# Kernel optimization log

Measured on AMD Instinct MI355X. Metric: run time of the kernel, lower is better.

The kernel has to match this reference:

```python
import jax, jax.numpy as jnp
import numpy as np

B, T, S, D, V = 8, 128, 400, 512, 50000
EPS_LN = 1e-6

def setup_inputs() -> dict:
    key = jax.random.key(0)
    ks = jax.random.split(key, 10)
    a = jax.random.uniform(ks[0], (B, T, S), dtype=jnp.float32)
    attn_weights = a / jnp.sum(a, axis=-1, keepdims=True)  # row-stochastic like softmax attention
    return {
        'x': jax.random.normal(ks[1], (B, T, D), dtype=jnp.float32),
        'x_t': jax.random.normal(ks[2], (B, T, D), dtype=jnp.float32),
        'memory': jax.random.normal(ks[3], (B, S, D), dtype=jnp.float32),
        'attn_weights': attn_weights,
        'src': jax.random.randint(ks[4], (B, S), 0, V),
        'norm_a': jnp.ones((D,), jnp.float32),
        'norm_b': jnp.zeros((D,), jnp.float32),
        'proj_w': jax.random.normal(ks[5], (V, D), dtype=jnp.float32) * (1.0 / np.sqrt(D)),
        'proj_b': jnp.zeros((V,), jnp.float32),
        'wh_w': jax.random.normal(ks[6], (1, D), dtype=jnp.float32) * (1.0 / np.sqrt(D)),
        'wh_b': jnp.zeros((1,), jnp.float32),
        'ws_w': jax.random.normal(ks[7], (1, D), dtype=jnp.float32) * (1.0 / np.sqrt(D)),
        'ws_b': jnp.zeros((1,), jnp.float32),
        'wx_w': jax.random.normal(ks[8], (1, D), dtype=jnp.float32) * (1.0 / np.sqrt(D)),
        'wx_b': jnp.zeros((1,), jnp.float32),
        'bptr': jnp.zeros((1, 1), jnp.float32),
    }

def _layer_norm(x, a, b):
    mu = jnp.mean(x, axis=-1, keepdims=True)
    sd = jnp.std(x, axis=-1, keepdims=True)
    return a * (x - mu) / (sd + EPS_LN) + b

def reference(x, x_t, memory, attn_weights, src, norm_a, norm_b, proj_w, proj_b,
              wh_w, wh_b, ws_w, ws_b, wx_w, wx_b, bptr):
    # generation distribution over vocab: [B,T,V]
    dec_dist = jnp.einsum('btd,vd->btv', _layer_norm(x, norm_a, norm_b), proj_w) + proj_b
    # context vector h_t = attn @ memory: [B,T,D]
    h_t = jnp.einsum('bts,bsd->btd', attn_weights, memory)
    # p_gen gate: [B,T,1]
    logits = (jnp.einsum('btd,od->bto', h_t, wh_w) + wh_b
              + jnp.einsum('btd,od->bto', x, ws_w) + ws_b
              + jnp.einsum('btd,od->bto', x_t, wx_w) + wx_b
              + bptr[0, 0])
    p_gen = jax.nn.sigmoid(logits)
    # copy distribution via scatter_add of attention mass onto source token ids
    b_idx = jnp.arange(B)[:, None, None]
    t_idx = jnp.arange(T)[None, :, None]
    v_idx = src[:, None, :]  # broadcast over T -> [B,T,S] index
    enc_attn_dist = jnp.zeros((B, T, V), dtype=dec_dist.dtype).at[b_idx, t_idx, v_idx].add(attn_weights)
    out = jnp.log(p_gen * jax.nn.softmax(dec_dist, axis=-1) + (1.0 - p_gen) * enc_attn_dist + 1e-12)
    return out, p_gen
```

## Files before the change

### kernel.cpp

```cpp
#include <hip/hip_runtime.h>
#include <hip/hip_bf16.h>
#include <cstdint>

#define B_  8
#define T_  128
#define S_  400
#define D_  512
#define V_  50000
#define M_  (B_*T_)
#define EPS_LN 1e-6f

typedef __bf16 bf16x8 __attribute__((ext_vector_type(8)));
typedef float  f32x4  __attribute__((ext_vector_type(4)));
typedef unsigned short u16;
typedef unsigned short u16x4 __attribute__((ext_vector_type(4)));
typedef unsigned short u16x8 __attribute__((ext_vector_type(8)));

__device__ __forceinline__ float bf2f(u16 u) {
    union { unsigned i; float f; } c; c.i = ((unsigned)u) << 16; return c.f;
}
__device__ __forceinline__ u16 f2bf(float f) {
    union { float f; unsigned i; } c; c.f = f;
    unsigned i = c.i;
    unsigned r = (i + 0x7FFFu + ((i >> 16) & 1u)) >> 16;
    return (u16)r;
}

__device__ __forceinline__ float bsum(float v, float* sb) {
    #pragma unroll
    for (int o = 32; o; o >>= 1) v += __shfl_xor(v, o);
    __syncthreads();
    if ((threadIdx.x & 63) == 0) sb[threadIdx.x >> 6] = v;
    __syncthreads();
    return sb[0] + sb[1] + sb[2] + sb[3];
}
__device__ __forceinline__ float bmax(float v, float* sb) {
    #pragma unroll
    for (int o = 32; o; o >>= 1) v = fmaxf(v, __shfl_xor(v, o));
    __syncthreads();
    if ((threadIdx.x & 63) == 0) sb[threadIdx.x >> 6] = v;
    __syncthreads();
    return fmaxf(fmaxf(sb[0], sb[1]), fmaxf(sb[2], sb[3]));
}

__global__ void k_mw(const float* __restrict__ mem, const float* __restrict__ wh,
                     float* __restrict__ mw) {
    __shared__ float sb[4];
    int row = blockIdx.x;
    const float* mr = mem + (size_t)row * D_;
    int t = threadIdx.x;
    float2 m2 = *(const float2*)(mr + t * 2);
    float2 w2 = *(const float2*)(wh + t * 2);
    float v = m2.x * w2.x + m2.y * w2.y;
    float tot = bsum(v, sb);
    if (t == 0) mw[row] = tot;
}

__global__ void k_wconv(const float* __restrict__ w, u16* __restrict__ wb) {
    size_t i = ((size_t)blockIdx.x * 256 + threadIdx.x) * 8;
    float4 a = *(const float4*)(w + i);
    float4 b = *(const float4*)(w + i + 4);
    u16x8 o;
    o[0] = f2bf(a.x); o[1] = f2bf(a.y); o[2] = f2bf(a.z); o[3] = f2bf(a.w);
    o[4] = f2bf(b.x); o[5] = f2bf(b.y); o[6] = f2bf(b.z); o[7] = f2bf(b.w);
    *(u16x8*)(wb + i) = o;
}

__global__ void k_rows(const float* __restrict__ x, const float* __restrict__ xt,
                       const float* __restrict__ attn, const float* __restrict__ mw,
                       const float* __restrict__ na, const float* __restrict__ nb,
                       const float* __restrict__ wsw, const float* __restrict__ wxw,
                       const float* __restrict__ whb, const float* __restrict__ wsb,
                       const float* __restrict__ wxb, const float* __restrict__ bp,
                       u16* __restrict__ Ab, float* __restrict__ pgen,
                       float* __restrict__ outp) {
    __shared__ float sb[4];
    int row = blockIdx.x;
    int b = row / T_;
    int tid = threadIdx.x;
    const float* xr  = x  + (size_t)row * D_;
    const float* xtr = xt + (size_t)row * D_;
    float2 xv = *(const float2*)(xr + tid * 2);
    float tsx  = bsum(xv.x + xv.y, sb);
    float tsx2 = bsum(xv.x * xv.x + xv.y * xv.y, sb);
    float mu  = tsx / (float)D_;
    float var = fmaxf(tsx2 / (float)D_ - mu * mu, 0.f);
    float rs  = 1.f / (sqrtf(var) + EPS_LN);
    float2 nav = *(const float2*)(na + tid * 2);
    float2 nbv = *(const float2*)(nb + tid * 2);
    u16 a0 = f2bf(nav.x * (xv.x - mu) * rs + nbv.x);
    u16 a1 = f2bf(nav.y * (xv.y - mu) * rs + nbv.y);
    ((unsigned*)(Ab + (size_t)row * D_))[tid] = (unsigned)a0 | ((unsigned)a1 << 16);
    float2 wsv = *(const float2*)(wsw + tid * 2);
    float2 wxv = *(const float2*)(wxw + tid * 2);
    float2 xtv = *(const float2*)(xtr + tid * 2);
    float dot = xv.x * wsv.x + xv.y * wsv.y + xtv.x * wxv.x + xtv.y * wxv.y;
    if (tid < 200) {
        const float* ar  = attn + (size_t)row * S_;
        const float* mwb = mw + b * S_;
        float2 av = *(const float2*)(ar + tid * 2);
        float2 mv = *(const float2*)(mwb + tid * 2);
        dot += av.x * mv.x + av.y * mv.y;
    }
    float tdot = bsum(dot, sb);
    if (tid == 0) {
        float logit = tdot + whb[0] + wsb[0] + wxb[0] + bp[0];
        float p = 1.f / (1.f + __expf(-logit));
        pgen[row] = p;
        outp[row] = p;
    }
}

__global__ __launch_bounds__(256) void k_gemm(const u16* __restrict__ Ab,
                                              const u16* __restrict__ Wb,
                                              const float* __restrict__ projb,
                                              u16* __restrict__ dec) {
    __shared__ __align__(16) u16 As[128 * 32];
    __shared__ __align__(16) u16 Bs[128 * 32];
    int bid = blockIdx.x;
    int xcd = bid & 7, loc = bid >> 3;
    int wg = xcd * 391 + loc;
    int mt = wg & 7, nt = wg >> 3;
    int brow = mt * 128, bcol = nt * 128;
    int tid = threadIdx.x, lane = tid & 63, wv = tid >> 6;
    int wm = wv >> 1, wn = wv & 1;
    int kq = lane >> 4, lr = lane & 15;
    f32x4 acc[4][4] = {};
    for (int kt = 0; kt < 16; ++kt) {
        #pragma unroll
        for (int i = 0; i < 2; ++i) {
            int flat = i * 4096 + tid * 16;
            int r = flat >> 6, kb = flat & 63;
            const u16* ga = Ab + (size_t)(brow + r) * 512 + kt * 32 + (kb >> 1);
            int vr = bcol + r; if (vr >= V_) vr = V_ - 1;
            const u16* gb = Wb + (size_t)vr * 512 + kt * 32 + (kb >> 1);
            __builtin_amdgcn_global_load_lds(
                (const __attribute__((address_space(1))) unsigned*)ga,
                (__attribute__((address_space(3))) unsigned*)((char*)As + flat), 16, 0, 0);
            __builtin_amdgcn_global_load_lds(
                (const __attribute__((address_space(1))) unsigned*)gb,
                (__attribute__((address_space(3))) unsigned*)((char*)Bs + flat), 16, 0, 0);
        }
        __syncthreads();
        bf16x8 af[4], bfr[4];
        const bf16x8* Afp = (const bf16x8*)As;
        const bf16x8* Bfp = (const bf16x8*)Bs;
        #pragma unroll
        for (int m = 0; m < 4; ++m) af[m]  = Afp[(wm * 64 + m * 16 + lr) * 4 + kq];
        #pragma unroll
        for (int n = 0; n < 4; ++n) bfr[n] = Bfp[(wn * 64 + n * 16 + lr) * 4 + kq];
        #pragma unroll
        for (int m = 0; m < 4; ++m)
            #pragma unroll
            for (int n = 0; n < 4; ++n)
                acc[m][n] = __builtin_amdgcn_mfma_f32_16x16x32_bf16(af[m], bfr[n], acc[m][n], 0, 0, 0);
        __syncthreads();
    }
    #pragma unroll
    for (int m = 0; m < 4; ++m) {
        int rbase = brow + wm * 64 + m * 16 + kq * 4;
        #pragma unroll
        for (int n = 0; n < 4; ++n) {
            int col = bcol + wn * 64 + n * 16 + lr;
            if (col < V_) {
                float pb = projb[col];
                #pragma unroll
                for (int i = 0; i < 4; ++i) {
                    int row = rbase + i;
                    dec[(size_t)row * V_ + col] = f2bf(acc[m][n][i] + pb);
                }
            }
        }
    }
}

__global__ void k_stats(const u16* __restrict__ dec, float* __restrict__ base) {
    __shared__ float sb[4];
    int row = blockIdx.x;
    const u16* dr = dec + (size_t)row * V_;
    int tid = threadIdx.x;
    float mx = -1e30f;
    for (int i0 = tid * 8; i0 < V_; i0 += 2048) {
        u16x8 v = *(const u16x8*)(dr + i0);
        #pragma unroll
        for (int j = 0; j < 8; ++j) mx = fmaxf(mx, bf2f(v[j]));
    }
    mx = bmax(mx, sb);
    float s = 0.f;
    for (int i0 = tid * 8; i0 < V_; i0 += 2048) {
        u16x8 v = *(const u16x8*)(dr + i0);
        #pragma unroll
        for (int j = 0; j < 8; ++j) s += __expf(bf2f(v[j]) - mx);
    }
    s = bsum(s, sb);
    if (tid == 0) base[row] = mx + __logf(s);
}

__global__ void k_final(const u16* __restrict__ dec, const float* __restrict__ pgen,
                        const float* __restrict__ base, float* __restrict__ out) {
    int row = blockIdx.y;
    int v0 = blockIdx.x * 1024 + threadIdx.x * 4;
    if (v0 >= V_) return;
    float p  = pgen[row];
    float bs = base[row];
    u16x4 d = *(const u16x4*)(dec + (size_t)row * V_ + v0);
    float4 o;
    o.x = __logf(p * __expf(bf2f(d[0]) - bs) + 1e-12f);
    o.y = __logf(p * __expf(bf2f(d[1]) - bs) + 1e-12f);
    o.z = __logf(p * __expf(bf2f(d[2]) - bs) + 1e-12f);
    o.w = __logf(p * __expf(bf2f(d[3]) - bs) + 1e-12f);
    *(float4*)(out + (size_t)row * V_ + v0) = o;
}

__global__ void k_fix(const int* __restrict__ src, const float* __restrict__ attn,
                      const u16* __restrict__ dec, const float* __restrict__ pgen,
                      const float* __restrict__ base, float* __restrict__ out) {
    int b = blockIdx.x / S_, s = blockIdx.x % S_;
    const int* sr = src + b * S_;
    int v = sr[s];
    for (int s2 = 0; s2 < s; ++s2)
        if (sr[s2] == v) return;
    int t = threadIdx.x;
    float enc = 0.f;
    const float* ar = attn + (size_t)(b * T_ + t) * S_;
    for (int s2 = s; s2 < S_; ++s2)
        if (sr[s2] == v) enc += ar[s2];
    int row = b * T_ + t;
    float p  = pgen[row];
    float bs = base[row];
    float d  = bf2f(dec[(size_t)row * V_ + v]);
    out[(size_t)row * V_ + v] = __logf(p * __expf(d - bs) + (1.f - p) * enc + 1e-12f);
}

extern "C" void kernel_launch(void* const* d_in, const int* in_sizes, int n_in,
                              void* d_out, int out_size, void* d_ws, size_t ws_size,
                              hipStream_t stream) {
    const float* x    = (const float*)d_in[0];
    const float* xt   = (const float*)d_in[1];
    const float* mem  = (const float*)d_in[2];
    const float* attn = (const float*)d_in[3];
    const int*   src  = (const int*)d_in[4];
    const float* na   = (const float*)d_in[5];
    const float* nb   = (const float*)d_in[6];
    const float* pw   = (const float*)d_in[7];
    const float* pb   = (const float*)d_in[8];
    const float* whw  = (const float*)d_in[9];
    const float* whb  = (const float*)d_in[10];
    const float* wsw  = (const float*)d_in[11];
    const float* wsb  = (const float*)d_in[12];
    const float* wxw  = (const float*)d_in[13];
    const float* wxb  = (const float*)d_in[14];
    const float* bp   = (const float*)d_in[15];

    char* ws = (char*)d_ws;
    u16*   Wb   = (u16*)(ws + 0);
    u16*   Ab   = (u16*)(ws + 51200000);
    u16*   dec  = (u16*)(ws + 52248576);
    float* mw   = (float*)(ws + 154648576);
    float* pgen = (float*)(ws + 154661376);
    float* base = (float*)(ws + 154665472);
    float* out  = (float*)d_out;
    float* outp = out + (size_t)M_ * V_;

    k_mw   <<<B_ * S_, 256, 0, stream>>>(mem, whw, mw);
    k_wconv<<<12500, 256, 0, stream>>>(pw, Wb);
    k_rows <<<M_, 256, 0, stream>>>(x, xt, attn, mw, na, nb, wsw, wxw,
                                    whb, wsb, wxb, bp, Ab, pgen, outp);
    k_gemm <<<3128, 256, 0, stream>>>(Ab, Wb, pb, dec);
    k_stats<<<M_, 256, 0, stream>>>(dec, base);
    k_final<<<dim3(49, M_), 256, 0, stream>>>(dec, pgen, base, out);
    k_fix  <<<B_ * S_, 128, 0, stream>>>(src, attn, dec, pgen, base, out);
}
```

Baseline: 276.5 us.

## Fuse softmax row stats into GEMM epilogue and swizzle LDS tile layout

The GEMM epilogue now computes per-row partial max and sum-of-exp for each 128-column tile and writes them to small workspace arrays. A tiny reduce kernel combines these partials into the log-sum-exp base, replacing the stats kernel that re-read the full bf16 logits twice. The LDS tile layout is also reordered so each MFMA fragment is a contiguous per-lane read, and the final kernel handles 8 elements per thread. This adds shuffles and exp work to the GEMM epilogue in exchange for removing a large memory pass.

```diff
diff --git a/kernel.cpp b/kernel.cpp
--- a/kernel.cpp
+++ b/kernel.cpp
@@ -8,12 +8,12 @@
 #define D_  512
 #define V_  50000
 #define M_  (B_*T_)
+#define NT_ 391
 #define EPS_LN 1e-6f
 
 typedef __bf16 bf16x8 __attribute__((ext_vector_type(8)));
 typedef float  f32x4  __attribute__((ext_vector_type(4)));
 typedef unsigned short u16;
-typedef unsigned short u16x4 __attribute__((ext_vector_type(4)));
 typedef unsigned short u16x8 __attribute__((ext_vector_type(8)));
 
 __device__ __forceinline__ float bf2f(u16 u) {
@@ -114,9 +114,13 @@
 __global__ __launch_bounds__(256) void k_gemm(const u16* __restrict__ Ab,
                                               const u16* __restrict__ Wb,
                                               const float* __restrict__ projb,
-                                              u16* __restrict__ dec) {
+                                              u16* __restrict__ dec,
+                                              float* __restrict__ pmax,
+                                              float* __restrict__ psum) {
     __shared__ __align__(16) u16 As[128 * 32];
     __shared__ __align__(16) u16 Bs[128 * 32];
+    __shared__ float smax[2][128];
+    __shared__ float ssum[2][128];
     int bid = blockIdx.x;
     int xcd = bid & 7, loc = bid >> 3;
     int wg = xcd * 391 + loc;
@@ -130,10 +134,13 @@
         #pragma unroll
         for (int i = 0; i < 2; ++i) {
             int flat = i * 4096 + tid * 16;
-            int r = flat >> 6, kb = flat & 63;
-            const u16* ga = Ab + (size_t)(brow + r) * 512 + kt * 32 + (kb >> 1);
-            int vr = bcol + r; if (vr >= V_) vr = V_ - 1;
-            const u16* gb = Wb + (size_t)vr * 512 + kt * 32 + (kb >> 1);
+            int sub = flat >> 10;
+            int l   = (flat >> 4) & 63;
+            int kq2 = l >> 4, lr2 = l & 15;
+            int arow = brow + sub * 16 + lr2;
+            const u16* ga = Ab + (size_t)arow * 512 + kt * 32 + kq2 * 8;
+            int vrow = bcol + sub * 16 + lr2; if (vrow >= V_) vrow = V_ - 1;
+            const u16* gb = Wb + (size_t)vrow * 512 + kt * 32 + kq2 * 8;
             __builtin_amdgcn_global_load_lds(
                 (const __attribute__((address_space(1))) unsigned*)ga,
                 (__attribute__((address_space(3))) unsigned*)((char*)As + flat), 16, 0, 0);
@@ -146,9 +153,9 @@
         const bf16x8* Afp = (const bf16x8*)As;
         const bf16x8* Bfp = (const bf16x8*)Bs;
         #pragma unroll
-        for (int m = 0; m < 4; ++m) af[m]  = Afp[(wm * 64 + m * 16 + lr) * 4 + kq];
-        #pragma unroll
-        for (int n = 0; n < 4; ++n) bfr[n] = Bfp[(wn * 64 + n * 16 + lr) * 4 + kq];
+        for (int m = 0; m < 4; ++m) af[m]  = Afp[(wm * 4 + m) * 64 + lane];
+        #pragma unroll
+        for (int n = 0; n < 4; ++n) bfr[n] = Bfp[(wn * 4 + n) * 64 + lane];
         #pragma unroll
         for (int m = 0; m < 4; ++m)
             #pragma unroll
@@ -156,60 +163,89 @@
                 acc[m][n] = __builtin_amdgcn_mfma_f32_16x16x32_bf16(af[m], bfr[n], acc[m][n], 0, 0, 0);
         __syncthreads();
     }
+    float pbn[4];
+    int   cval[4];
+    #pragma unroll
+    for (int n = 0; n < 4; ++n) {
+        int col = bcol + wn * 64 + n * 16 + lr;
+        cval[n] = (col < V_);
+        pbn[n]  = cval[n] ? projb[col] : 0.f;
+    }
     #pragma unroll
     for (int m = 0; m < 4; ++m) {
-        int rbase = brow + wm * 64 + m * 16 + kq * 4;
-        #pragma unroll
-        for (int n = 0; n < 4; ++n) {
-            int col = bcol + wn * 64 + n * 16 + lr;
-            if (col < V_) {
-                float pb = projb[col];
-                #pragma unroll
-                for (int i = 0; i < 4; ++i) {
-                    int row = rbase + i;
-                    dec[(size_t)row * V_ + col] = f2bf(acc[m][n][i] + pb);
+        #pragma unroll
+        for (int i = 0; i < 4; ++i) {
+            int row128 = wm * 64 + m * 16 + kq * 4 + i;
+            int grow = brow + row128;
+            float dv[4];
+            float mx = -1e30f;
+            #pragma unroll
+            for (int n = 0; n < 4; ++n) {
+                dv[n] = cval[n] ? acc[m][n][i] + pbn[n] : -1e30f;
+                mx = fmaxf(mx, dv[n]);
+            }
+            #pragma unroll
+            for (int o = 1; o < 16; o <<= 1) mx = fmaxf(mx, __shfl_xor(mx, o));
+            float se = 0.f;
+            #pragma unroll
+            for (int n = 0; n < 4; ++n) {
+                if (cval[n]) {
+                    se += __expf(dv[n] - mx);
+                    dec[(size_t)grow * V_ + (bcol + wn * 64 + n * 16 + lr)] = f2bf(dv[n]);
                 }
             }
+            #pragma unroll
+            for (int o = 1; o < 16; o <<= 1) se += __shfl_xor(se, o);
+            if (lr == 0) { smax[wn][row128] = mx; ssum[wn][row128] = se; }
         }
     }
-}
-
-__global__ void k_stats(const u16* __restrict__ dec, float* __restrict__ base) {
+    __syncthreads();
+    if (tid < 128) {
+        float m0 = smax[0][tid], m1 = smax[1][tid];
+        float M = fmaxf(m0, m1);
+        float S = ssum[0][tid] * __expf(m0 - M) + ssum[1][tid] * __expf(m1 - M);
+        size_t idx = (size_t)(brow + tid) * NT_ + nt;
+        pmax[idx] = M;
+        psum[idx] = S;
+    }
+}
+
+__global__ void k_reduce(const float* __restrict__ pmax, const float* __restrict__ psum,
+                         float* __restrict__ base) {
     __shared__ float sb[4];
     int row = blockIdx.x;
-    const u16* dr = dec + (size_t)row * V_;
-    int tid = threadIdx.x;
+    int t = threadIdx.x;
+    const float* pm = pmax + (size_t)row * NT_;
+    const float* ps = psum + (size_t)row * NT_;
     float mx = -1e30f;
-    for (int i0 = tid * 8; i0 < V_; i0 += 2048) {
-        u16x8 v = *(const u16x8*)(dr + i0);
-        #pragma unroll
-        for (int j = 0; j < 8; ++j) mx = fmaxf(mx, bf2f(v[j]));
-    }
+    for (int j = t; j < NT_; j += 256) mx = fmaxf(mx, pm[j]);
     mx = bmax(mx, sb);
     float s = 0.f;
-    for (int i0 = tid * 8; i0 < V_; i0 += 2048) {
-        u16x8 v = *(const u16x8*)(dr + i0);
-        #pragma unroll
-        for (int j = 0; j < 8; ++j) s += __expf(bf2f(v[j]) - mx);
-    }
+    for (int j = t; j < NT_; j += 256) s += ps[j] * __expf(pm[j] - mx);
     s = bsum(s, sb);
-    if (tid == 0) base[row] = mx + __logf(s);
+    if (t == 0) base[row] = mx + __logf(s);
 }
 
 __global__ void k_final(const u16* __restrict__ dec, const float* __restrict__ pgen,
                         const float* __restrict__ base, float* __restrict__ out) {
     int row = blockIdx.y;
-    int v0 = blockIdx.x * 1024 + threadIdx.x * 4;
+    int v0 = (blockIdx.x * 256 + threadIdx.x) * 8;
     if (v0 >= V_) return;
     float p  = pgen[row];
     float bs = base[row];
-    u16x4 d = *(const u16x4*)(dec + (size_t)row * V_ + v0);
-    float4 o;
-    o.x = __logf(p * __expf(bf2f(d[0]) - bs) + 1e-12f);
-    o.y = __logf(p * __expf(bf2f(d[1]) - bs) + 1e-12f);
-    o.z = __logf(p * __expf(bf2f(d[2]) - bs) + 1e-12f);
-    o.w = __logf(p * __expf(bf2f(d[3]) - bs) + 1e-12f);
-    *(float4*)(out + (size_t)row * V_ + v0) = o;
+    u16x8 d = *(const u16x8*)(dec + (size_t)row * V_ + v0);
+    float4 o0, o1;
+    o0.x = __logf(p * __expf(bf2f(d[0]) - bs) + 1e-12f);
+    o0.y = __logf(p * __expf(bf2f(d[1]) - bs) + 1e-12f);
+    o0.z = __logf(p * __expf(bf2f(d[2]) - bs) + 1e-12f);
+    o0.w = __logf(p * __expf(bf2f(d[3]) - bs) + 1e-12f);
+    o1.x = __logf(p * __expf(bf2f(d[4]) - bs) + 1e-12f);
+    o1.y = __logf(p * __expf(bf2f(d[5]) - bs) + 1e-12f);
+    o1.z = __logf(p * __expf(bf2f(d[6]) - bs) + 1e-12f);
+    o1.w = __logf(p * __expf(bf2f(d[7]) - bs) + 1e-12f);
+    float* op = out + (size_t)row * V_ + v0;
+    *(float4*)op = o0;
+    *(float4*)(op + 4) = o1;
 }
 
 __global__ void k_fix(const int* __restrict__ src, const float* __restrict__ attn,
@@ -256,18 +292,20 @@
     u16*   Wb   = (u16*)(ws + 0);
     u16*   Ab   = (u16*)(ws + 51200000);
     u16*   dec  = (u16*)(ws + 52248576);
-    float* mw   = (float*)(ws + 154648576);
-    float* pgen = (float*)(ws + 154661376);
-    float* base = (float*)(ws + 154665472);
+    float* pmax = (float*)(ws + 154648576);
+    float* psum = (float*)(ws + 156250112);
+    float* mw   = (float*)(ws + 157851648);
+    float* pgen = (float*)(ws + 157864448);
+    float* base = (float*)(ws + 157868544);
     float* out  = (float*)d_out;
     float* outp = out + (size_t)M_ * V_;
 
-    k_mw   <<<B_ * S_, 256, 0, stream>>>(mem, whw, mw);
-    k_wconv<<<12500, 256, 0, stream>>>(pw, Wb);
-    k_rows <<<M_, 256, 0, stream>>>(x, xt, attn, mw, na, nb, wsw, wxw,
-                                    whb, wsb, wxb, bp, Ab, pgen, outp);
-    k_gemm <<<3128, 256, 0, stream>>>(Ab, Wb, pb, dec);
-    k_stats<<<M_, 256, 0, stream>>>(dec, base);
-    k_final<<<dim3(49, M_), 256, 0, stream>>>(dec, pgen, base, out);
-    k_fix  <<<B_ * S_, 128, 0, stream>>>(src, attn, dec, pgen, base, out);
-}
+    k_mw    <<<B_ * S_, 256, 0, stream>>>(mem, whw, mw);
+    k_wconv <<<12500, 256, 0, stream>>>(pw, Wb);
+    k_rows  <<<M_, 256, 0, stream>>>(x, xt, attn, mw, na, nb, wsw, wxw,
+                                     whb, wsb, wxb, bp, Ab, pgen, outp);
+    k_gemm  <<<3128, 256, 0, stream>>>(Ab, Wb, pb, dec, pmax, psum);
+    k_reduce<<<M_, 256, 0, stream>>>(pmax, psum, base);
+    k_final <<<dim3(25, M_), 256, 0, stream>>>(dec, pgen, base, out);
+    k_fix   <<<B_ * S_, 128, 0, stream>>>(src, attn, dec, pgen, base, out);
+}
```

After: 303.2 us. 9.7% more time.
